# Performance work log

Hardware: AMD Instinct MI355X
Metric: run time of the kernel (lower is better)

Reference implementation:

```python
import jax, jax.numpy as jnp
import numpy as np

N_NODES = 500000
N_EDGES = 16000000
IN_DIM = 17


def setup_inputs() -> dict:
    key = jax.random.key(0)
    k1, k2, k3, k4, k5, k6, k7 = jax.random.split(key, 7)
    x = jax.random.normal(k1, (N_NODES, IN_DIM), dtype=jnp.float32)
    edge_index = jax.random.randint(k2, (2, N_EDGES), 0, N_NODES, dtype=jnp.int64)
    edge_weight = jax.random.uniform(k3, (N_EDGES,), dtype=jnp.float32)
    # SAGEConv(17, 1): lin_l applied to aggregated neighbors (with bias),
    # lin_r applied to root features (no bias, PyG convention).
    s = 1.0 / np.sqrt(IN_DIM)
    w_l = jax.random.uniform(k4, (1, IN_DIM), minval=-s, maxval=s, dtype=jnp.float32)
    b_l = jax.random.uniform(k5, (1,), minval=-s, maxval=s, dtype=jnp.float32)
    w_r = jax.random.uniform(k6, (1, IN_DIM), minval=-s, maxval=s, dtype=jnp.float32)
    # out: Linear(1, 1)
    k8, k9 = jax.random.split(k7)
    w_o = jax.random.uniform(k8, (1, 1), minval=-1.0, maxval=1.0, dtype=jnp.float32)
    b_o = jax.random.uniform(k9, (1,), minval=-1.0, maxval=1.0, dtype=jnp.float32)
    return {"x": x, "edge_index": edge_index, "edge_weight": edge_weight,
            "w_l": w_l, "b_l": b_l, "w_r": w_r, "w_o": w_o, "b_o": b_o}


def reference(x, edge_index, edge_weight, w_l, b_l, w_r, w_o, b_o):
    # SAGEConv (mean aggregation). edge_weight is unused (faithful to PyG SAGEConv).
    # Project to out_dim=1 BEFORE aggregation (linearity makes this exact and
    # avoids materializing a [E,17] gathered buffer):
    #   lin_l(mean_j x_j) + b_l == mean_j (x_j @ W_l^T) + b_l
    src, dst = edge_index[0], edge_index[1]
    x_proj_l = x @ w_l.T                      # [N, 1]
    msg = x_proj_l[src, 0]                    # [E]  gathered source projections
    agg = jax.ops.segment_sum(msg, dst, num_segments=x.shape[0])          # [N]
    cnt = jax.ops.segment_sum(jnp.ones_like(msg), dst, num_segments=x.shape[0])
    mean = agg / jnp.maximum(cnt, 1.0)        # zero for isolated nodes
    h = mean[:, None] + b_l + x @ w_r.T       # [N, 1]  lin_l(aggr) + lin_r(x)
    h = jax.nn.elu(h)
    return h @ w_o.T + b_o                    # [N, 1]
```

## Files before the change

### kernel.cpp

```cpp
#include <hip/hip_runtime.h>
#include <hip/hip_bf16.h>
#include <math.h>

#define IN_DIM 17
#define NB 128
#define LOG_BN 12
#define BN 4096
#define K_SPLIT 16
#define CHUNK 8192
#define EPT 32
#define VAL_SCALE 4096.0f
#define FP_SCALE 268435456.0f
#define FP_INV   (1.0 / 268435456.0)

__global__ void node_proj_kernel(const float* __restrict__ x,
                                 const float* __restrict__ w_l,
                                 const float* __restrict__ w_r,
                                 float* __restrict__ p_l,
                                 float* __restrict__ p_r,
                                 int n_nodes) {
    int i = blockIdx.x * blockDim.x + threadIdx.x;
    if (i >= n_nodes) return;
    const float* row = x + (size_t)i * IN_DIM;
    float sl = 0.0f, sr = 0.0f;
#pragma unroll
    for (int k = 0; k < IN_DIM; ++k) {
        float v = row[k];
        sl = fmaf(v, w_l[k], sl);
        sr = fmaf(v, w_r[k], sr);
    }
    p_l[i] = sl;
    p_r[i] = sr;
}

__global__ __launch_bounds__(256, 4)
void sort_scatter_kernel(const int* __restrict__ src,
                         const int* __restrict__ dst,
                         const float* __restrict__ p_l,
                         unsigned* __restrict__ staging,
                         unsigned short* __restrict__ segtab,
                         int n_edges) {
    __shared__ unsigned cnt[NB];
    __shared__ unsigned sstart[NB + 1];
    __shared__ unsigned lbuf[CHUNK];

    const int tid = threadIdx.x;
    const int blk = blockIdx.x;
    const int e0 = blk * CHUNK;
    const int chunk_n = min(CHUNK, n_edges - e0);
    const int nvec = chunk_n >> 2;

    for (int t = tid; t < NB; t += 256) cnt[t] = 0;
    __syncthreads();

    uint4 dreg[EPT / 4];
    uint4 sreg[EPT / 4];
    unsigned rpack[EPT / 2];
    const uint4* dv = (const uint4*)(dst + e0);
    const uint4* sv = (const uint4*)(src + e0);
#pragma unroll
    for (int k = 0; k < EPT / 4; ++k) {
        int q = tid + k * 256;
        if (q < nvec) {
            uint4 d = dv[q];
            dreg[k] = d;
            sreg[k] = sv[q];
            unsigned r0 = atomicAdd(&cnt[d.x >> LOG_BN], 1u);
            unsigned r1 = atomicAdd(&cnt[d.y >> LOG_BN], 1u);
            unsigned r2 = atomicAdd(&cnt[d.z >> LOG_BN], 1u);
            unsigned r3 = atomicAdd(&cnt[d.w >> LOG_BN], 1u);
            rpack[2 * k]     = r0 | (r1 << 16);
            rpack[2 * k + 1] = r2 | (r3 << 16);
        }
    }
    unsigned tail_rank = 0;
    {
        int i = (nvec << 2) + tid;
        if (i < chunk_n)
            tail_rank = atomicAdd(&cnt[(unsigned)dst[e0 + i] >> LOG_BN], 1u);
    }
    __syncthreads();

    if (tid < 64) {
        unsigned c0 = cnt[tid], c1 = cnt[tid + 64];
        unsigned s0 = c0;
#pragma unroll
        for (int off = 1; off < 64; off <<= 1) {
            unsigned v = __shfl_up(s0, off);
            if (tid >= off) s0 += v;
        }
        unsigned tot0 = __shfl(s0, 63);
        unsigned s1 = c1;
#pragma unroll
        for (int off = 1; off < 64; off <<= 1) {
            unsigned v = __shfl_up(s1, off);
            if (tid >= off) s1 += v;
        }
        s1 += tot0;
        sstart[tid + 1] = s0;
        sstart[tid + 65] = s1;
        if (tid == 0) sstart[0] = 0;
    }
    __syncthreads();

    for (int t = tid; t <= NB; t += 256)
        segtab[(size_t)blk * (NB + 2) + t] = (unsigned short)sstart[t];

#pragma unroll
    for (int k = 0; k < EPT / 4; ++k) {
        int q = tid + k * 256;
        if (q < nvec) {
            uint4 s = sreg[k];
            uint4 d = dreg[k];
            float pf[4] = {p_l[s.x], p_l[s.y], p_l[s.z], p_l[s.w]};
            unsigned dd[4] = {d.x, d.y, d.z, d.w};
            unsigned rk[4] = {rpack[2 * k] & 0xFFFFu, rpack[2 * k] >> 16,
                              rpack[2 * k + 1] & 0xFFFFu, rpack[2 * k + 1] >> 16};
#pragma unroll
            for (int u = 0; u < 4; ++u) {
                int fx = __float2int_rn(pf[u] * VAL_SCALE);
                fx = max(-32768, min(32767, fx));
                unsigned entry = ((unsigned)(fx & 0xFFFF) << 16) | (dd[u] & (BN - 1));
                unsigned b = dd[u] >> LOG_BN;
                lbuf[sstart[b] + rk[u]] = entry;
            }
        }
    }
    {
        int i = (nvec << 2) + tid;
        if (i < chunk_n) {
            unsigned s = (unsigned)src[e0 + i];
            unsigned d = (unsigned)dst[e0 + i];
            int fx = __float2int_rn(p_l[s] * VAL_SCALE);
            fx = max(-32768, min(32767, fx));
            unsigned entry = ((unsigned)(fx & 0xFFFF) << 16) | (d & (BN - 1));
            lbuf[sstart[d >> LOG_BN] + tail_rank] = entry;
        }
    }
    __syncthreads();

    uint4* outp = (uint4*)(staging + (size_t)blk * CHUNK);
    const uint4* lp = (const uint4*)lbuf;
    int nv4 = (chunk_n + 3) >> 2;
    for (int q = tid; q < nv4; q += 256)
        outp[q] = lp[q];
}

__global__ __launch_bounds__(256, 8)
void reduce_kernel(const unsigned* __restrict__ staging,
                   const unsigned short* __restrict__ segtab,
                   unsigned* __restrict__ partials,
                   int nblk) {
    __shared__ unsigned lds_p[BN];
    const int tid = threadIdx.x;
    const int b = blockIdx.x / K_SPLIT;
    const int j = blockIdx.x % K_SPLIT;
    const int wave = tid >> 6, lane = tid & 63;

    for (int i = tid; i < BN; i += 256) lds_p[i] = 0u;
    __syncthreads();

    const int blk0 = (int)((long long)nblk * j / K_SPLIT);
    const int blk1 = (int)((long long)nblk * (j + 1) / K_SPLIT);

    int blk = blk0 + wave;
    unsigned s_nxt = 0, e_nxt = 0;
    if (blk < blk1) {
        const unsigned short* st = segtab + (size_t)blk * (NB + 2) + b;
        s_nxt = st[0];
        e_nxt = st[1];
    }
    while (blk < blk1) {
        unsigned s = s_nxt, e = e_nxt;
        const int nxt = blk + 4;
        if (nxt < blk1) {
            const unsigned short* st = segtab + (size_t)nxt * (NB + 2) + b;
            s_nxt = st[0];
            e_nxt = st[1];
        }
        const unsigned* sp = staging + (size_t)blk * CHUNK;
        for (unsigned i = s + lane; i < e; i += 64) {
            unsigned en = sp[i];
            int v = (int)(short)(en >> 16);
            atomicAdd(&lds_p[en & (BN - 1)], ((unsigned)v << 8) | 1u);
        }
        blk = nxt;
    }
    __syncthreads();
    size_t out_base = (size_t)blockIdx.x * BN;
    for (int i = tid; i < BN; i += 256)
        partials[out_base + i] = lds_p[i];
}

__global__ void finalize_kernel(const float* __restrict__ p_r,
                                const unsigned* __restrict__ partials,
                                const float* __restrict__ b_l,
                                const float* __restrict__ w_o,
                                const float* __restrict__ b_o,
                                float* __restrict__ out,
                                int n_nodes) {
    int i = blockIdx.x * blockDim.x + threadIdx.x;
    if (i >= n_nodes) return;
    int b = i >> LOG_BN;
    int loc = i & (BN - 1);
    int sum24 = 0, cnt = 0;
#pragma unroll
    for (int j = 0; j < K_SPLIT; ++j) {
        unsigned u = partials[((size_t)b * K_SPLIT + j) * BN + loc];
        sum24 += ((int)u) >> 8;
        cnt += (int)(u & 0xFFu);
    }
    float sum = (float)sum24 * (1.0f / VAL_SCALE);
    float mean = sum / fmaxf((float)cnt, 1.0f);
    float h = mean + b_l[0] + p_r[i];
    h = (h > 0.0f) ? h : expm1f(h);
    out[i] = fmaf(h, w_o[0], b_o[0]);
}

__global__ void edge_scatter_fb(const int* __restrict__ edge_index,
                                const float* __restrict__ p_l,
                                unsigned long long* __restrict__ bins,
                                int n_edges) {
    int e = blockIdx.x * blockDim.x + threadIdx.x;
    if (e >= n_edges) return;
    int s = edge_index[e];
    int d = edge_index[n_edges + e];
    float p = p_l[s];
    long long sfx = (long long)llrintf(p * FP_SCALE);
    unsigned long long delta = ((unsigned long long)sfx << 20) | 1ULL;
    atomicAdd(&bins[d], delta);
}

__global__ void finalize_fb(const float* __restrict__ p_r,
                            const unsigned long long* __restrict__ bins,
                            const float* __restrict__ b_l,
                            const float* __restrict__ w_o,
                            const float* __restrict__ b_o,
                            float* __restrict__ out,
                            int n_nodes) {
    int i = blockIdx.x * blockDim.x + threadIdx.x;
    if (i >= n_nodes) return;
    long long packed = (long long)bins[i];
    int cntv = (int)(packed & 0xFFFFFLL);
    long long sfx = packed >> 20;
    float sum = (float)((double)sfx * FP_INV);
    float mean = sum / fmaxf((float)cntv, 1.0f);
    float h = mean + b_l[0] + p_r[i];
    h = (h > 0.0f) ? h : expm1f(h);
    out[i] = fmaf(h, w_o[0], b_o[0]);
}

static inline size_t align_up(size_t v, size_t a) { return (v + a - 1) & ~(a - 1); }

extern "C" void kernel_launch(void* const* d_in, const int* in_sizes, int n_in,
                              void* d_out, int out_size, void* d_ws, size_t ws_size,
                              hipStream_t stream) {
    const float* x   = (const float*)d_in[0];
    const int*   ei  = (const int*)d_in[1];
    const float* w_l = (const float*)d_in[3];
    const float* b_l = (const float*)d_in[4];
    const float* w_r = (const float*)d_in[5];
    const float* w_o = (const float*)d_in[6];
    const float* b_o = (const float*)d_in[7];
    float* out = (float*)d_out;

    const int n_nodes = in_sizes[0] / IN_DIM;
    const int n_edges = in_sizes[2];
    const int* src = ei;
    const int* dst = ei + n_edges;
    const int nblk = (n_edges + CHUNK - 1) / CHUNK;

    char* ws = (char*)d_ws;
    size_t off = 0;
    size_t o_pl = off;      off = align_up(off + (size_t)n_nodes * 4, 256);
    size_t o_pr = off;      off = align_up(off + (size_t)n_nodes * 4, 256);
    size_t o_stage = off;   off = align_up(off + (size_t)nblk * CHUNK * 4, 256);
    size_t o_seg = off;     off = align_up(off + (size_t)nblk * (NB + 2) * 2, 256);
    size_t o_part = off;    off = align_up(off + (size_t)NB * K_SPLIT * BN * 4, 256);
    size_t need = off;

    float* p_l = (float*)(ws + o_pl);
    float* p_r = (float*)(ws + o_pr);

    const int B = 256;
    node_proj_kernel<<<(n_nodes + B - 1) / B, B, 0, stream>>>(x, w_l, w_r, p_l, p_r, n_nodes);

    if (ws_size >= need) {
        unsigned* staging       = (unsigned*)(ws + o_stage);
        unsigned short* segtab  = (unsigned short*)(ws + o_seg);
        unsigned* partials      = (unsigned*)(ws + o_part);

        sort_scatter_kernel<<<nblk, B, 0, stream>>>(src, dst, p_l, staging, segtab, n_edges);
        reduce_kernel<<<NB * K_SPLIT, B, 0, stream>>>(staging, segtab, partials, nblk);
        finalize_kernel<<<(n_nodes + B - 1) / B, B, 0, stream>>>(p_r, partials, b_l, w_o, b_o,
                                                                 out, n_nodes);
    } else {
        unsigned long long* bins = (unsigned long long*)(ws + o_stage);
        hipMemsetAsync(bins, 0, (size_t)n_nodes * 8, stream);
        edge_scatter_fb<<<(n_edges + B - 1) / B, B, 0, stream>>>(ei, p_l, bins, n_edges);
        finalize_fb<<<(n_nodes + B - 1) / B, B, 0, stream>>>(p_r, bins, b_l, w_o, b_o,
                                                             out, n_nodes);
    }
}
```

Baseline: 343.1 us.

## Halve sort chunk, gather projections early, and split reduce waves into half-waves

The sort/scatter kernel now processes 4096-edge chunks at higher occupancy. It gathers and quantizes the p_l source projections during the counting phase, so those random loads overlap the LDS atomic histogram instead of following the scan. The reduce kernel assigns each half-wave its own staging block, which suits the smaller per-bucket segments produced by smaller chunks. The costs are twice as many blocks and segtab entries, and more partially idle lanes on short segments.

```diff
diff --git a/kernel.cpp b/kernel.cpp
--- a/kernel.cpp
+++ b/kernel.cpp
@@ -7,8 +7,8 @@
 #define LOG_BN 12
 #define BN 4096
 #define K_SPLIT 16
-#define CHUNK 8192
-#define EPT 32
+#define CHUNK 4096
+#define EPT 16
 #define VAL_SCALE 4096.0f
 #define FP_SCALE 268435456.0f
 #define FP_INV   (1.0 / 268435456.0)
@@ -33,7 +33,7 @@
     p_r[i] = sr;
 }
 
-__global__ __launch_bounds__(256, 4)
+__global__ __launch_bounds__(256, 8)
 void sort_scatter_kernel(const int* __restrict__ src,
                          const int* __restrict__ dst,
                          const float* __restrict__ p_l,
@@ -54,8 +54,8 @@
     __syncthreads();
 
     uint4 dreg[EPT / 4];
-    uint4 sreg[EPT / 4];
-    unsigned rpack[EPT / 2];
+    unsigned fxpack[EPT / 2];
+    unsigned rkpack[EPT / 2];
     const uint4* dv = (const uint4*)(dst + e0);
     const uint4* sv = (const uint4*)(src + e0);
 #pragma unroll
@@ -63,80 +63,83 @@
         int q = tid + k * 256;
         if (q < nvec) {
             uint4 d = dv[q];
+            uint4 s = sv[q];
             dreg[k] = d;
-            sreg[k] = sv[q];
+            float pf0 = p_l[s.x], pf1 = p_l[s.y], pf2 = p_l[s.z], pf3 = p_l[s.w];
             unsigned r0 = atomicAdd(&cnt[d.x >> LOG_BN], 1u);
             unsigned r1 = atomicAdd(&cnt[d.y >> LOG_BN], 1u);
             unsigned r2 = atomicAdd(&cnt[d.z >> LOG_BN], 1u);
             unsigned r3 = atomicAdd(&cnt[d.w >> LOG_BN], 1u);
-            rpack[2 * k]     = r0 | (r1 << 16);
-            rpack[2 * k + 1] = r2 | (r3 << 16);
-        }
-    }
-    unsigned tail_rank = 0;
-    {
-        int i = (nvec << 2) + tid;
-        if (i < chunk_n)
-            tail_rank = atomicAdd(&cnt[(unsigned)dst[e0 + i] >> LOG_BN], 1u);
-    }
-    __syncthreads();
-
-    if (tid < 64) {
-        unsigned c0 = cnt[tid], c1 = cnt[tid + 64];
-        unsigned s0 = c0;
-#pragma unroll
-        for (int off = 1; off < 64; off <<= 1) {
-            unsigned v = __shfl_up(s0, off);
-            if (tid >= off) s0 += v;
-        }
-        unsigned tot0 = __shfl(s0, 63);
-        unsigned s1 = c1;
-#pragma unroll
-        for (int off = 1; off < 64; off <<= 1) {
-            unsigned v = __shfl_up(s1, off);
-            if (tid >= off) s1 += v;
-        }
-        s1 += tot0;
-        sstart[tid + 1] = s0;
-        sstart[tid + 65] = s1;
-        if (tid == 0) sstart[0] = 0;
-    }
-    __syncthreads();
-
-    for (int t = tid; t <= NB; t += 256)
-        segtab[(size_t)blk * (NB + 2) + t] = (unsigned short)sstart[t];
-
-#pragma unroll
-    for (int k = 0; k < EPT / 4; ++k) {
-        int q = tid + k * 256;
-        if (q < nvec) {
-            uint4 s = sreg[k];
-            uint4 d = dreg[k];
-            float pf[4] = {p_l[s.x], p_l[s.y], p_l[s.z], p_l[s.w]};
-            unsigned dd[4] = {d.x, d.y, d.z, d.w};
-            unsigned rk[4] = {rpack[2 * k] & 0xFFFFu, rpack[2 * k] >> 16,
-                              rpack[2 * k + 1] & 0xFFFFu, rpack[2 * k + 1] >> 16};
-#pragma unroll
-            for (int u = 0; u < 4; ++u) {
-                int fx = __float2int_rn(pf[u] * VAL_SCALE);
-                fx = max(-32768, min(32767, fx));
-                unsigned entry = ((unsigned)(fx & 0xFFFF) << 16) | (dd[u] & (BN - 1));
-                unsigned b = dd[u] >> LOG_BN;
-                lbuf[sstart[b] + rk[u]] = entry;
-            }
-        }
-    }
+            int f0 = max(-32768, min(32767, __float2int_rn(pf0 * VAL_SCALE)));
+            int f1 = max(-32768, min(32767, __float2int_rn(pf1 * VAL_SCALE)));
+            int f2 = max(-32768, min(32767, __float2int_rn(pf2 * VAL_SCALE)));
+            int f3 = max(-32768, min(32767, __float2int_rn(pf3 * VAL_SCALE)));
+            fxpack[2 * k]     = ((unsigned)f0 & 0xFFFFu) | ((unsigned)f1 << 16);
+            fxpack[2 * k + 1] = ((unsigned)f2 & 0xFFFFu) | ((unsigned)f3 << 16);
+            rkpack[2 * k]     = r0 | (r1 << 16);
+            rkpack[2 * k + 1] = r2 | (r3 << 16);
+        }
+    }
+    unsigned tail_rank = 0, tail_entry = 0, tail_b = 0;
+    int tail_valid = 0;
     {
         int i = (nvec << 2) + tid;
         if (i < chunk_n) {
             unsigned s = (unsigned)src[e0 + i];
             unsigned d = (unsigned)dst[e0 + i];
-            int fx = __float2int_rn(p_l[s] * VAL_SCALE);
-            fx = max(-32768, min(32767, fx));
-            unsigned entry = ((unsigned)(fx & 0xFFFF) << 16) | (d & (BN - 1));
-            lbuf[sstart[d >> LOG_BN] + tail_rank] = entry;
-        }
-    }
+            int fx = max(-32768, min(32767, __float2int_rn(p_l[s] * VAL_SCALE)));
+            tail_entry = ((unsigned)(fx & 0xFFFF) << 16) | (d & (BN - 1));
+            tail_b = d >> LOG_BN;
+            tail_rank = atomicAdd(&cnt[tail_b], 1u);
+            tail_valid = 1;
+        }
+    }
+    __syncthreads();
+
+    if (tid < 64) {
+        unsigned c0 = cnt[tid], c1 = cnt[tid + 64];
+        unsigned s0 = c0;
+#pragma unroll
+        for (int off = 1; off < 64; off <<= 1) {
+            unsigned v = __shfl_up(s0, off);
+            if (tid >= off) s0 += v;
+        }
+        unsigned tot0 = __shfl(s0, 63);
+        unsigned s1 = c1;
+#pragma unroll
+        for (int off = 1; off < 64; off <<= 1) {
+            unsigned v = __shfl_up(s1, off);
+            if (tid >= off) s1 += v;
+        }
+        s1 += tot0;
+        sstart[tid + 1] = s0;
+        sstart[tid + 65] = s1;
+        if (tid == 0) sstart[0] = 0;
+    }
+    __syncthreads();
+
+    for (int t = tid; t <= NB; t += 256)
+        segtab[(size_t)blk * (NB + 2) + t] = (unsigned short)sstart[t];
+
+#pragma unroll
+    for (int k = 0; k < EPT / 4; ++k) {
+        int q = tid + k * 256;
+        if (q < nvec) {
+            uint4 d = dreg[k];
+            unsigned dd[4] = {d.x, d.y, d.z, d.w};
+            unsigned fb[4] = {fxpack[2 * k] & 0xFFFFu, fxpack[2 * k] >> 16,
+                              fxpack[2 * k + 1] & 0xFFFFu, fxpack[2 * k + 1] >> 16};
+            unsigned rk[4] = {rkpack[2 * k] & 0xFFFFu, rkpack[2 * k] >> 16,
+                              rkpack[2 * k + 1] & 0xFFFFu, rkpack[2 * k + 1] >> 16};
+#pragma unroll
+            for (int u = 0; u < 4; ++u) {
+                unsigned entry = (fb[u] << 16) | (dd[u] & (BN - 1));
+                lbuf[sstart[dd[u] >> LOG_BN] + rk[u]] = entry;
+            }
+        }
+    }
+    if (tail_valid)
+        lbuf[sstart[tail_b] + tail_rank] = tail_entry;
     __syncthreads();
 
     uint4* outp = (uint4*)(staging + (size_t)blk * CHUNK);
@@ -155,7 +158,9 @@
     const int tid = threadIdx.x;
     const int b = blockIdx.x / K_SPLIT;
     const int j = blockIdx.x % K_SPLIT;
-    const int wave = tid >> 6, lane = tid & 63;
+    const int wave = tid >> 6;
+    const int half = (tid >> 5) & 1;
+    const int lane32 = tid & 31;
 
     for (int i = tid; i < BN; i += 256) lds_p[i] = 0u;
     __syncthreads();
@@ -163,28 +168,30 @@
     const int blk0 = (int)((long long)nblk * j / K_SPLIT);
     const int blk1 = (int)((long long)nblk * (j + 1) / K_SPLIT);
 
-    int blk = blk0 + wave;
+    int cur = blk0 + wave * 2 + half;
     unsigned s_nxt = 0, e_nxt = 0;
-    if (blk < blk1) {
-        const unsigned short* st = segtab + (size_t)blk * (NB + 2) + b;
+    if (cur < blk1) {
+        const unsigned short* st = segtab + (size_t)cur * (NB + 2) + b;
         s_nxt = st[0];
         e_nxt = st[1];
     }
-    while (blk < blk1) {
+    for (int base = blk0 + wave * 2; base < blk1; base += 8) {
+        const int myblk = base + half;
         unsigned s = s_nxt, e = e_nxt;
-        const int nxt = blk + 4;
+        const int nxt = myblk + 8;
         if (nxt < blk1) {
             const unsigned short* st = segtab + (size_t)nxt * (NB + 2) + b;
             s_nxt = st[0];
             e_nxt = st[1];
-        }
-        const unsigned* sp = staging + (size_t)blk * CHUNK;
-        for (unsigned i = s + lane; i < e; i += 64) {
+        } else {
+            s_nxt = 0; e_nxt = 0;
+        }
+        const unsigned* sp = staging + (size_t)myblk * CHUNK;
+        for (unsigned i = s + lane32; i < e; i += 32) {
             unsigned en = sp[i];
             int v = (int)(short)(en >> 16);
             atomicAdd(&lds_p[en & (BN - 1)], ((unsigned)v << 8) | 1u);
         }
-        blk = nxt;
     }
     __syncthreads();
     size_t out_base = (size_t)blockIdx.x * BN;
```

Result: slower. 351.8 us (+2.5%).

## Prefetch staging entries two blocks ahead and merge partials with global atomics

Applied to the files above, without the earlier changes.

The reduce kernel now software-pipelines its loop: the segment bounds for block+8 and the first two staging entries for block+4 are loaded into registers before the current block's LDS atomics run, which hides global load latency. Instead of writing K_SPLIT separate partial histograms and summing them in finalize, each block atomically adds its nonzero LDS bins into one zeroed global bin array, and finalize reads a single value per node. This removes the partials write/read traffic and the 16-way gather in finalize, at the cost of an extra memset, global atomic contention, and more register pressure.

```diff
diff --git a/kernel.cpp b/kernel.cpp
--- a/kernel.cpp
+++ b/kernel.cpp
@@ -149,7 +149,7 @@
 __global__ __launch_bounds__(256, 8)
 void reduce_kernel(const unsigned* __restrict__ staging,
                    const unsigned short* __restrict__ segtab,
-                   unsigned* __restrict__ partials,
+                   unsigned* __restrict__ bins,
                    int nblk) {
     __shared__ unsigned lds_p[BN];
     const int tid = threadIdx.x;
@@ -164,36 +164,73 @@
     const int blk1 = (int)((long long)nblk * (j + 1) / K_SPLIT);
 
     int blk = blk0 + wave;
-    unsigned s_nxt = 0, e_nxt = 0;
+
+    unsigned sA = 0, eA = 0, sB = 0, eB = 0;
+    unsigned enA0 = 0, enA1 = 0;
     if (blk < blk1) {
         const unsigned short* st = segtab + (size_t)blk * (NB + 2) + b;
-        s_nxt = st[0];
-        e_nxt = st[1];
-    }
+        sA = st[0]; eA = st[1];
+    }
+    if (blk + 4 < blk1) {
+        const unsigned short* st = segtab + (size_t)(blk + 4) * (NB + 2) + b;
+        sB = st[0]; eB = st[1];
+    }
+    if (blk < blk1) {
+        const unsigned* sp = staging + (size_t)blk * CHUNK;
+        unsigned i0 = sA + lane;
+        if (i0 < eA) enA0 = sp[i0];
+        unsigned i1 = i0 + 64;
+        if (i1 < eA) enA1 = sp[i1];
+    }
+
     while (blk < blk1) {
-        unsigned s = s_nxt, e = e_nxt;
-        const int nxt = blk + 4;
-        if (nxt < blk1) {
-            const unsigned short* st = segtab + (size_t)nxt * (NB + 2) + b;
-            s_nxt = st[0];
-            e_nxt = st[1];
-        }
-        const unsigned* sp = staging + (size_t)blk * CHUNK;
-        for (unsigned i = s + lane; i < e; i += 64) {
-            unsigned en = sp[i];
-            int v = (int)(short)(en >> 16);
-            atomicAdd(&lds_p[en & (BN - 1)], ((unsigned)v << 8) | 1u);
-        }
-        blk = nxt;
-    }
-    __syncthreads();
-    size_t out_base = (size_t)blockIdx.x * BN;
-    for (int i = tid; i < BN; i += 256)
-        partials[out_base + i] = lds_p[i];
+        unsigned sC = 0, eC = 0;
+        if (blk + 8 < blk1) {
+            const unsigned short* st = segtab + (size_t)(blk + 8) * (NB + 2) + b;
+            sC = st[0]; eC = st[1];
+        }
+        unsigned enB0 = 0, enB1 = 0;
+        if (blk + 4 < blk1) {
+            const unsigned* spn = staging + (size_t)(blk + 4) * CHUNK;
+            unsigned i0 = sB + lane;
+            if (i0 < eB) enB0 = spn[i0];
+            unsigned i1 = i0 + 64;
+            if (i1 < eB) enB1 = spn[i1];
+        }
+        {
+            unsigned i0 = sA + lane;
+            if (i0 < eA) {
+                int v = (int)(short)(enA0 >> 16);
+                atomicAdd(&lds_p[enA0 & (BN - 1)], ((unsigned)v << 8) | 1u);
+            }
+            unsigned i1 = i0 + 64;
+            if (i1 < eA) {
+                int v = (int)(short)(enA1 >> 16);
+                atomicAdd(&lds_p[enA1 & (BN - 1)], ((unsigned)v << 8) | 1u);
+            }
+            if (sA + 128 < eA) {
+                const unsigned* sp = staging + (size_t)blk * CHUNK;
+                for (unsigned i = sA + 128 + lane; i < eA; i += 64) {
+                    unsigned en = sp[i];
+                    int v = (int)(short)(en >> 16);
+                    atomicAdd(&lds_p[en & (BN - 1)], ((unsigned)v << 8) | 1u);
+                }
+            }
+        }
+        blk += 4;
+        sA = sB; eA = eB; enA0 = enB0; enA1 = enB1;
+        sB = sC; eB = eC;
+    }
+    __syncthreads();
+    unsigned* gb = bins + (size_t)b * BN;
+    for (int i = tid; i < BN; i += 256) {
+        unsigned v = lds_p[i];
+        if (v) atomicAdd(&gb[i], v);
+    }
 }
 
 __global__ void finalize_kernel(const float* __restrict__ p_r,
-                                const unsigned* __restrict__ partials,
+                                const unsigned* __restrict__ bins,
                                 const float* __restrict__ b_l,
                                 const float* __restrict__ w_o,
                                 const float* __restrict__ b_o,
@@ -201,15 +238,9 @@
                                 int n_nodes) {
     int i = blockIdx.x * blockDim.x + threadIdx.x;
     if (i >= n_nodes) return;
-    int b = i >> LOG_BN;
-    int loc = i & (BN - 1);
-    int sum24 = 0, cnt = 0;
-#pragma unroll
-    for (int j = 0; j < K_SPLIT; ++j) {
-        unsigned u = partials[((size_t)b * K_SPLIT + j) * BN + loc];
-        sum24 += ((int)u) >> 8;
-        cnt += (int)(u & 0xFFu);
-    }
+    unsigned u = bins[i];
+    int sum24 = ((int)u) >> 8;
+    int cnt = (int)(u & 0xFFu);
     float sum = (float)sum24 * (1.0f / VAL_SCALE);
     float mean = sum / fmaxf((float)cnt, 1.0f);
     float h = mean + b_l[0] + p_r[i];
@@ -276,7 +307,7 @@
     size_t o_pr = off;      off = align_up(off + (size_t)n_nodes * 4, 256);
     size_t o_stage = off;   off = align_up(off + (size_t)nblk * CHUNK * 4, 256);
     size_t o_seg = off;     off = align_up(off + (size_t)nblk * (NB + 2) * 2, 256);
-    size_t o_part = off;    off = align_up(off + (size_t)NB * K_SPLIT * BN * 4, 256);
+    size_t o_bins = off;    off = align_up(off + (size_t)NB * BN * 4, 256);
     size_t need = off;
 
     float* p_l = (float*)(ws + o_pl);
@@ -288,11 +319,12 @@
     if (ws_size >= need) {
         unsigned* staging       = (unsigned*)(ws + o_stage);
         unsigned short* segtab  = (unsigned short*)(ws + o_seg);
-        unsigned* partials      = (unsigned*)(ws + o_part);
-
+        unsigned* bins          = (unsigned*)(ws + o_bins);
+
+        hipMemsetAsync(bins, 0, (size_t)NB * BN * 4, stream);
         sort_scatter_kernel<<<nblk, B, 0, stream>>>(src, dst, p_l, staging, segtab, n_edges);
-        reduce_kernel<<<NB * K_SPLIT, B, 0, stream>>>(staging, segtab, partials, nblk);
-        finalize_kernel<<<(n_nodes + B - 1) / B, B, 0, stream>>>(p_r, partials, b_l, w_o, b_o,
+        reduce_kernel<<<NB * K_SPLIT, B, 0, stream>>>(staging, segtab, bins, nblk);
+        finalize_kernel<<<(n_nodes + B - 1) / B, B, 0, stream>>>(p_r, bins, b_l, w_o, b_o,
                                                                  out, n_nodes);
     } else {
         unsigned long long* bins = (unsigned long long*)(ws + o_stage);
```

New measurement: 347.7 us. About the same (+1.3%).
